# Performance work log

Hardware: AMD Instinct MI355X
Metric: run time of the kernel (lower is better)

Reference implementation:

```python
import jax, jax.numpy as jnp
import numpy as np

IN_F, OUT_F, NG = 2048, 8192, 16
EPS = 1e-5

def setup_inputs() -> dict:
    key = jax.random.key(0)
    k = jax.random.split(key, 6)
    x = jax.random.normal(k[0], (4096, IN_F), dtype=jnp.float32)
    W = jax.random.normal(k[1], (OUT_F, IN_F), dtype=jnp.float32) * (1.0 / np.sqrt(IN_F))
    b = jax.random.normal(k[2], (OUT_F,), dtype=jnp.float32) * 0.01
    gn_w = jnp.ones((OUT_F,), dtype=jnp.float32)
    gn_b = jnp.zeros((OUT_F,), dtype=jnp.float32)
    mult_w = jax.random.normal(k[3], (OUT_F,), dtype=jnp.float32)
    return {"x": x, "W": W, "b": b, "gn_w": gn_w, "gn_b": gn_b, "mult_w": mult_w}

def reference(x, W, b, gn_w, gn_b, mult_w):
    B = x.shape[0]
    y = x @ W.T + b  # [B, OUT_F]
    g = y.reshape(B, NG, OUT_F // NG)
    mean = jnp.mean(g, axis=-1, keepdims=True)
    var = jnp.mean(jnp.square(g - mean), axis=-1, keepdims=True)
    n = ((g - mean) * jax.lax.rsqrt(var + EPS)).reshape(B, OUT_F)
    n = n * gn_w + gn_b
    s1 = n * jax.nn.sigmoid(n)
    m = s1 * mult_w
    return m * jax.nn.sigmoid(m)
```

## Files before the change

### kernel.cpp

```cpp
#include <hip/hip_runtime.h>

#define M_DIM 4096
#define N_DIM 8192
#define K_DIM 2048
#define NGRP 16
#define GSZ 512
#define EPSV 1e-5f

#define NX (M_DIM * K_DIM)
#define NW (N_DIM * K_DIM)
#define NY ((size_t)M_DIM * N_DIM)

typedef __attribute__((ext_vector_type(8))) short bf16x8;
typedef __attribute__((ext_vector_type(4))) float f32x4;
typedef __attribute__((ext_vector_type(8))) short shortx8;

__device__ __forceinline__ float b2f(short u) {
    union { unsigned u32; float f; } c;
    c.u32 = ((unsigned)(unsigned short)u) << 16;
    return c.f;
}

__device__ __forceinline__ short f2b(float f) {
    union { float f; unsigned u; } c; c.f = f;
    unsigned r = (c.u + 0x7fffu + ((c.u >> 16) & 1u)) >> 16;
    return (short)r;
}

__global__ __launch_bounds__(256) void convert_kernel(
    const float* __restrict__ x, const float* __restrict__ W,
    short* __restrict__ dst)
{
    const size_t base = ((size_t)blockIdx.x * 256 + threadIdx.x) * 32;
    const float* src = (base < NX) ? (x + base) : (W + (base - NX));
    f32x4 v[8];
#pragma unroll
    for (int c = 0; c < 8; ++c) v[c] = *(const f32x4*)(src + c * 4);
#pragma unroll
    for (int c = 0; c < 4; ++c) {
        shortx8 o;
#pragma unroll
        for (int j = 0; j < 4; ++j) {
            o[j]     = f2b(v[2 * c][j]);
            o[j + 4] = f2b(v[2 * c + 1][j]);
        }
        *(shortx8*)(dst + base + c * 8) = o;
    }
}

#define BKS 32
#define NTILES (K_DIM / BKS)

__global__ __launch_bounds__(512, 2) void gemm256_bf16_kernel(
    const short* __restrict__ A, const short* __restrict__ W, short* __restrict__ C)
{
    __shared__ __align__(16) short lds[4 * 16384];

    const int tid  = threadIdx.x;
    const int lane = tid & 63;
    const int wave = tid >> 6;
    const int wr   = wave >> 2;
    const int wc   = wave & 3;
    const int blockRow = blockIdx.y * 256;
    const int blockCol = blockIdx.x * 256;

    const int q0 = tid, q1 = tid + 512;
    const int sr0 = q0 >> 2, sc0 = (q0 & 3) ^ (sr0 & 3);
    const int sr1 = q1 >> 2, sc1 = (q1 & 3) ^ (sr1 & 3);
    const short* gA0 = A + (size_t)(blockRow + sr0) * K_DIM + sc0 * 8;
    const short* gA1 = A + (size_t)(blockRow + sr1) * K_DIM + sc1 * 8;
    const short* gB0 = W + (size_t)(blockCol + sr0) * K_DIM + sc0 * 8;
    const short* gB1 = W + (size_t)(blockCol + sr1) * K_DIM + sc1 * 8;

    const int fr    = lane & 15;
    const int pbyte = ((lane >> 4) ^ (fr & 3)) * 16;
    const int aBase = (wr * 128 + fr) * 64 + pbyte;
    const int bBase = (wc * 64  + fr) * 64 + pbyte;

    f32x4 acc[8][4] = {};

    auto stageT = [&](int t) {
        short* dA = lds + (t & 3) * 16384;
        short* dB = dA + 8192;
        const int ko = t * BKS;
        __builtin_amdgcn_global_load_lds(
            (const __attribute__((address_space(1))) void*)(gA0 + ko),
            (__attribute__((address_space(3))) void*)(dA + q0 * 8), 16, 0, 0);
        __builtin_amdgcn_global_load_lds(
            (const __attribute__((address_space(1))) void*)(gB0 + ko),
            (__attribute__((address_space(3))) void*)(dB + q0 * 8), 16, 0, 0);
        __builtin_amdgcn_global_load_lds(
            (const __attribute__((address_space(1))) void*)(gA1 + ko),
            (__attribute__((address_space(3))) void*)(dA + q1 * 8), 16, 0, 0);
        __builtin_amdgcn_global_load_lds(
            (const __attribute__((address_space(1))) void*)(gB1 + ko),
            (__attribute__((address_space(3))) void*)(dB + q1 * 8), 16, 0, 0);
    };

    stageT(0); stageT(1); stageT(2);

    for (int t = 0; t < NTILES; ++t) {
        __builtin_amdgcn_s_barrier();
        __builtin_amdgcn_sched_barrier(0);
        if (t + 3 < NTILES) {
            stageT(t + 3);
            asm volatile("s_waitcnt vmcnt(12)" ::: "memory");
        } else if (t + 2 < NTILES) {
            asm volatile("s_waitcnt vmcnt(8)" ::: "memory");
        } else if (t + 1 < NTILES) {
            asm volatile("s_waitcnt vmcnt(4)" ::: "memory");
        } else {
            asm volatile("s_waitcnt vmcnt(0)" ::: "memory");
        }
        __builtin_amdgcn_s_barrier();
        __builtin_amdgcn_sched_barrier(0);

        const char* bufA = (const char*)lds + (t & 3) * 32768;
        const char* bufB = bufA + 16384;
        bf16x8 af[8], bfv[4];
#pragma unroll
        for (int i = 0; i < 8; ++i)
            af[i] = *(const bf16x8*)(bufA + aBase + i * 1024);
#pragma unroll
        for (int j = 0; j < 4; ++j)
            bfv[j] = *(const bf16x8*)(bufB + bBase + j * 1024);

        __builtin_amdgcn_s_setprio(1);
#pragma unroll
        for (int i = 0; i < 8; ++i)
#pragma unroll
            for (int j = 0; j < 4; ++j)
                acc[i][j] = __builtin_amdgcn_mfma_f32_16x16x32_bf16(
                    af[i], bfv[j], acc[i][j], 0, 0, 0);
        __builtin_amdgcn_s_setprio(0);
    }

    const int er = (lane >> 4) * 4;
    const int ec = lane & 15;
#pragma unroll
    for (int i = 0; i < 8; ++i) {
        const int rr = blockRow + wr * 128 + i * 16 + er;
#pragma unroll
        for (int j = 0; j < 4; ++j) {
            const int cc = blockCol + wc * 64 + j * 16 + ec;
#pragma unroll
            for (int r = 0; r < 4; ++r)
                C[(size_t)(rr + r) * N_DIM + cc] = f2b(acc[i][j][r]);
        }
    }
}

__global__ __launch_bounds__(256) void gn_silu_bf16_kernel(
    const short* __restrict__ Y,
    const float* __restrict__ bias,
    const float* __restrict__ gnw,
    const float* __restrict__ gnb,
    const float* __restrict__ mw,
    float* __restrict__ out)
{
    const int lane = threadIdx.x & 63;
    const int wave = threadIdx.x >> 6;
    const unsigned gid = blockIdx.x * 4u + wave;
    const unsigned row = gid >> 4;
    const unsigned grp = gid & 15;
    const int col = grp * GSZ + lane * 8;
    const size_t off = (size_t)row * N_DIM + col;

    bf16x8 v = *(const bf16x8*)(Y + off);
    f32x4 b0 = *(const f32x4*)(bias + col);
    f32x4 b1 = *(const f32x4*)(bias + col + 4);

    float y[8];
    float s = 0.f, s2 = 0.f;
#pragma unroll
    for (int j = 0; j < 8; ++j) {
        y[j] = b2f(v[j]) + (j < 4 ? b0[j] : b1[j - 4]);
        s  += y[j];
        s2 += y[j] * y[j];
    }
#pragma unroll
    for (int d = 1; d < 64; d <<= 1) {
        s  += __shfl_xor(s,  d, 64);
        s2 += __shfl_xor(s2, d, 64);
    }
    const float mean = s * (1.0f / GSZ);
    const float var  = s2 * (1.0f / GSZ) - mean * mean;
    const float inv  = rsqrtf(var + EPSV);

    f32x4 w0 = *(const f32x4*)(gnw + col);
    f32x4 w1 = *(const f32x4*)(gnw + col + 4);
    f32x4 g0 = *(const f32x4*)(gnb + col);
    f32x4 g1 = *(const f32x4*)(gnb + col + 4);
    f32x4 m0 = *(const f32x4*)(mw + col);
    f32x4 m1 = *(const f32x4*)(mw + col + 4);

    f32x4 o0, o1;
#pragma unroll
    for (int j = 0; j < 8; ++j) {
        float gwv = j < 4 ? w0[j] : w1[j - 4];
        float gbv = j < 4 ? g0[j] : g1[j - 4];
        float mwv = j < 4 ? m0[j] : m1[j - 4];
        float n  = (y[j] - mean) * inv * gwv + gbv;
        float s1 = n / (1.f + __expf(-n));
        float m  = s1 * mwv;
        float r  = m / (1.f + __expf(-m));
        if (j < 4) o0[j] = r; else o1[j - 4] = r;
    }
    *(f32x4*)(out + off)     = o0;
    *(f32x4*)(out + off + 4) = o1;
}

__global__ __launch_bounds__(256) void gemm_bt_f32_kernel(
    const float* __restrict__ A, const float* __restrict__ W, float* __restrict__ C)
{
    __shared__ __align__(16) short ldsA[128 * 32];
    __shared__ __align__(16) short ldsB[128 * 32];

    const int tid  = threadIdx.x;
    const int lane = tid & 63;
    const int wave = tid >> 6;
    const int blockRow = blockIdx.y * 128;
    const int blockCol = blockIdx.x * 128;
    const int srow = tid >> 1;
    const int scol = (tid & 1) * 16;
    const int wm  = (wave >> 1) * 64;
    const int wn  = (wave & 1) * 64;
    const int fr  = lane & 15;
    const int fko = (lane >> 4) * 8;

    f32x4 acc[4][4] = {};
    const size_t aRowOff = (size_t)(blockRow + srow) * K_DIM;
    const size_t wRowOff = (size_t)(blockCol + srow) * K_DIM;

    for (int k0 = 0; k0 < K_DIM; k0 += 32) {
        f32x4 va0 = *(const f32x4*)(A + aRowOff + k0 + scol);
        f32x4 va1 = *(const f32x4*)(A + aRowOff + k0 + scol + 4);
        f32x4 va2 = *(const f32x4*)(A + aRowOff + k0 + scol + 8);
        f32x4 va3 = *(const f32x4*)(A + aRowOff + k0 + scol + 12);
        f32x4 vb0 = *(const f32x4*)(W + wRowOff + k0 + scol);
        f32x4 vb1 = *(const f32x4*)(W + wRowOff + k0 + scol + 4);
        f32x4 vb2 = *(const f32x4*)(W + wRowOff + k0 + scol + 8);
        f32x4 vb3 = *(const f32x4*)(W + wRowOff + k0 + scol + 12);
        bf16x8 a0, a1, b0, b1;
#pragma unroll
        for (int j = 0; j < 4; ++j) {
            a0[j] = f2b(va0[j]); a0[j + 4] = f2b(va1[j]);
            a1[j] = f2b(va2[j]); a1[j + 4] = f2b(va3[j]);
            b0[j] = f2b(vb0[j]); b0[j + 4] = f2b(vb1[j]);
            b1[j] = f2b(vb2[j]); b1[j + 4] = f2b(vb3[j]);
        }
        *(bf16x8*)(ldsA + srow * 32 + scol)     = a0;
        *(bf16x8*)(ldsA + srow * 32 + scol + 8) = a1;
        *(bf16x8*)(ldsB + srow * 32 + scol)     = b0;
        *(bf16x8*)(ldsB + srow * 32 + scol + 8) = b1;
        __syncthreads();

        bf16x8 af[4], bfv[4];
#pragma unroll
        for (int i = 0; i < 4; ++i) {
            af[i]  = *(const bf16x8*)(ldsA + (wm + i * 16 + fr) * 32 + fko);
            bfv[i] = *(const bf16x8*)(ldsB + (wn + i * 16 + fr) * 32 + fko);
        }
#pragma unroll
        for (int i = 0; i < 4; ++i)
#pragma unroll
            for (int j = 0; j < 4; ++j)
                acc[i][j] = __builtin_amdgcn_mfma_f32_16x16x32_bf16(
                    af[i], bfv[j], acc[i][j], 0, 0, 0);
        __syncthreads();
    }

    const int er = (lane >> 4) * 4;
    const int ec = lane & 15;
#pragma unroll
    for (int i = 0; i < 4; ++i) {
        const int r0 = blockRow + wm + i * 16 + er;
#pragma unroll
        for (int j = 0; j < 4; ++j) {
            const int c0 = blockCol + wn + j * 16 + ec;
#pragma unroll
            for (int r = 0; r < 4; ++r)
                C[(size_t)(r0 + r) * N_DIM + c0] = acc[i][j][r];
        }
    }
}

__global__ __launch_bounds__(256) void gn_silu_f32_kernel(
    float* __restrict__ Y,
    const float* __restrict__ bias,
    const float* __restrict__ gnw,
    const float* __restrict__ gnb,
    const float* __restrict__ mw)
{
    const int lane = threadIdx.x & 63;
    const int wave = threadIdx.x >> 6;
    const unsigned gid = blockIdx.x * 4u + wave;
    const unsigned row = gid >> 4;
    const unsigned grp = gid & 15;
    const int col = grp * GSZ + lane * 8;
    const size_t off = (size_t)row * N_DIM + col;

    f32x4 v0 = *(const f32x4*)(Y + off);
    f32x4 v1 = *(const f32x4*)(Y + off + 4);
    f32x4 b0 = *(const f32x4*)(bias + col);
    f32x4 b1 = *(const f32x4*)(bias + col + 4);

    float y[8];
    float s = 0.f, s2 = 0.f;
#pragma unroll
    for (int j = 0; j < 8; ++j) {
        y[j] = (j < 4 ? v0[j] + b0[j] : v1[j - 4] + b1[j - 4]);
        s += y[j]; s2 += y[j] * y[j];
    }
#pragma unroll
    for (int d = 1; d < 64; d <<= 1) {
        s  += __shfl_xor(s,  d, 64);
        s2 += __shfl_xor(s2, d, 64);
    }
    const float mean = s * (1.0f / GSZ);
    const float var  = s2 * (1.0f / GSZ) - mean * mean;
    const float inv  = rsqrtf(var + EPSV);

    f32x4 w0 = *(const f32x4*)(gnw + col);
    f32x4 w1 = *(const f32x4*)(gnw + col + 4);
    f32x4 g0 = *(const f32x4*)(gnb + col);
    f32x4 g1 = *(const f32x4*)(gnb + col + 4);
    f32x4 m0 = *(const f32x4*)(mw + col);
    f32x4 m1 = *(const f32x4*)(mw + col + 4);

    f32x4 o0, o1;
#pragma unroll
    for (int j = 0; j < 8; ++j) {
        float gwv = j < 4 ? w0[j] : w1[j - 4];
        float gbv = j < 4 ? g0[j] : g1[j - 4];
        float mwv = j < 4 ? m0[j] : m1[j - 4];
        float n  = (y[j] - mean) * inv * gwv + gbv;
        float s1 = n / (1.f + __expf(-n));
        float m  = s1 * mwv;
        float r  = m / (1.f + __expf(-m));
        if (j < 4) o0[j] = r; else o1[j - 4] = r;
    }
    *(f32x4*)(Y + off)     = o0;
    *(f32x4*)(Y + off + 4) = o1;
}

extern "C" void kernel_launch(void* const* d_in, const int* in_sizes, int n_in,
                              void* d_out, int out_size, void* d_ws, size_t ws_size,
                              hipStream_t stream)
{
    const float* x   = (const float*)d_in[0];
    const float* W   = (const float*)d_in[1];
    const float* b   = (const float*)d_in[2];
    const float* gnw = (const float*)d_in[3];
    const float* gnb = (const float*)d_in[4];
    const float* mw  = (const float*)d_in[5];
    float* out = (float*)d_out;

    const size_t need = ((size_t)NX + NW + NY) * sizeof(short);
    const int ngroups = M_DIM * NGRP;

    if (ws_size >= need) {
        short* xb = (short*)d_ws;
        short* Wb = xb + NX;
        short* yb = Wb + NW;

        convert_kernel<<<(NX + NW) / (256 * 32), 256, 0, stream>>>(x, W, xb);
        dim3 g256(N_DIM / 256, M_DIM / 256);
        gemm256_bf16_kernel<<<g256, 512, 0, stream>>>(xb, Wb, yb);
        gn_silu_bf16_kernel<<<ngroups / 4, 256, 0, stream>>>(yb, b, gnw, gnb, mw, out);
    } else {
        dim3 ggrid(N_DIM / 128, M_DIM / 128);
        gemm_bt_f32_kernel<<<ggrid, 256, 0, stream>>>(x, W, out);
        gn_silu_f32_kernel<<<ngroups / 4, 256, 0, stream>>>(out, b, gnw, gnb, mw);
    }
}
```

Before: 381.4 us.

## Double-buffer MFMA fragments in registers and retune LDS swizzle in bf16 GEMM

The K-loop now prefetches the next tile's A/B fragments from LDS into a second register set while MFMAs run on the current set. It ping-pongs between two 12-fragment buffers, with adjusted vmcnt/lgkmcnt waits and barriers. The LDS XOR swizzle now uses a row>>1 pattern on both the global-to-LDS write side and the fragment read side, aimed at reducing bank conflicts. Global addressing switches from precomputed pointers to 32-bit offsets. This hides LDS read latency behind MFMA work, at the cost of roughly 12 extra vector registers per thread, which may pressure occupancy at launch_bounds(512,2).

```diff
diff --git a/kernel.cpp b/kernel.cpp
--- a/kernel.cpp
+++ b/kernel.cpp
@@ -65,15 +65,15 @@
     const int blockCol = blockIdx.x * 256;
 
     const int q0 = tid, q1 = tid + 512;
-    const int sr0 = q0 >> 2, sc0 = (q0 & 3) ^ (sr0 & 3);
-    const int sr1 = q1 >> 2, sc1 = (q1 & 3) ^ (sr1 & 3);
-    const short* gA0 = A + (size_t)(blockRow + sr0) * K_DIM + sc0 * 8;
-    const short* gA1 = A + (size_t)(blockRow + sr1) * K_DIM + sc1 * 8;
-    const short* gB0 = W + (size_t)(blockCol + sr0) * K_DIM + sc0 * 8;
-    const short* gB1 = W + (size_t)(blockCol + sr1) * K_DIM + sc1 * 8;
+    const int sr0 = q0 >> 2, sc0 = (q0 & 3) ^ ((q0 >> 3) & 3);
+    const int sr1 = q1 >> 2, sc1 = (q1 & 3) ^ ((q1 >> 3) & 3);
+    const int offA0 = (blockRow + sr0) * K_DIM + sc0 * 8;
+    const int offA1 = (blockRow + sr1) * K_DIM + sc1 * 8;
+    const int offB0 = (blockCol + sr0) * K_DIM + sc0 * 8;
+    const int offB1 = (blockCol + sr1) * K_DIM + sc1 * 8;
 
     const int fr    = lane & 15;
-    const int pbyte = ((lane >> 4) ^ (fr & 3)) * 16;
+    const int pbyte = ((lane >> 4) ^ ((fr >> 1) & 3)) * 16;
     const int aBase = (wr * 128 + fr) * 64 + pbyte;
     const int bBase = (wc * 64  + fr) * 64 + pbyte;
 
@@ -84,55 +84,75 @@
         short* dB = dA + 8192;
         const int ko = t * BKS;
         __builtin_amdgcn_global_load_lds(
-            (const __attribute__((address_space(1))) void*)(gA0 + ko),
+            (const __attribute__((address_space(1))) void*)(A + offA0 + ko),
             (__attribute__((address_space(3))) void*)(dA + q0 * 8), 16, 0, 0);
         __builtin_amdgcn_global_load_lds(
-            (const __attribute__((address_space(1))) void*)(gB0 + ko),
+            (const __attribute__((address_space(1))) void*)(W + offB0 + ko),
             (__attribute__((address_space(3))) void*)(dB + q0 * 8), 16, 0, 0);
         __builtin_amdgcn_global_load_lds(
-            (const __attribute__((address_space(1))) void*)(gA1 + ko),
+            (const __attribute__((address_space(1))) void*)(A + offA1 + ko),
             (__attribute__((address_space(3))) void*)(dA + q1 * 8), 16, 0, 0);
         __builtin_amdgcn_global_load_lds(
-            (const __attribute__((address_space(1))) void*)(gB1 + ko),
+            (const __attribute__((address_space(1))) void*)(W + offB1 + ko),
             (__attribute__((address_space(3))) void*)(dB + q1 * 8), 16, 0, 0);
     };
 
-    stageT(0); stageT(1); stageT(2);
-
-    for (int t = 0; t < NTILES; ++t) {
+    auto ldfrags = [&](int t, bf16x8 (&f)[12]) {
+        const char* bufA = (const char*)lds + (t & 3) * 32768;
+        const char* bufB = bufA + 16384;
+#pragma unroll
+        for (int i = 0; i < 8; ++i)
+            f[i] = *(const bf16x8*)(bufA + aBase + i * 1024);
+#pragma unroll
+        for (int j = 0; j < 4; ++j)
+            f[8 + j] = *(const bf16x8*)(bufB + bBase + j * 1024);
+    };
+
+    auto domfma = [&](bf16x8 (&f)[12]) {
+        __builtin_amdgcn_s_setprio(1);
+#pragma unroll
+        for (int i = 0; i < 8; ++i)
+#pragma unroll
+            for (int j = 0; j < 4; ++j)
+                acc[i][j] = __builtin_amdgcn_mfma_f32_16x16x32_bf16(
+                    f[i], f[8 + j], acc[i][j], 0, 0, 0);
+        __builtin_amdgcn_s_setprio(0);
+    };
+
+    auto step = [&](int t, bf16x8 (&cur)[12], bf16x8 (&nxt)[12]) {
+        if (t + 3 < NTILES) {
+            stageT(t + 3);
+            asm volatile("s_waitcnt vmcnt(8)" ::: "memory");
+        } else if (t + 2 < NTILES) {
+            asm volatile("s_waitcnt vmcnt(4)" ::: "memory");
+        } else if (t + 1 < NTILES) {
+            asm volatile("s_waitcnt vmcnt(0)" ::: "memory");
+        }
         __builtin_amdgcn_s_barrier();
         __builtin_amdgcn_sched_barrier(0);
-        if (t + 3 < NTILES) {
-            stageT(t + 3);
-            asm volatile("s_waitcnt vmcnt(12)" ::: "memory");
-        } else if (t + 2 < NTILES) {
-            asm volatile("s_waitcnt vmcnt(8)" ::: "memory");
-        } else if (t + 1 < NTILES) {
-            asm volatile("s_waitcnt vmcnt(4)" ::: "memory");
+        if (t + 1 < NTILES) {
+            ldfrags(t + 1, nxt);
+            asm volatile("s_waitcnt lgkmcnt(12)" ::: "memory");
         } else {
-            asm volatile("s_waitcnt vmcnt(0)" ::: "memory");
-        }
+            asm volatile("s_waitcnt lgkmcnt(0)" ::: "memory");
+        }
+        __builtin_amdgcn_sched_barrier(0);
         __builtin_amdgcn_s_barrier();
         __builtin_amdgcn_sched_barrier(0);
-
-        const char* bufA = (const char*)lds + (t & 3) * 32768;
-        const char* bufB = bufA + 16384;
-        bf16x8 af[8], bfv[4];
-#pragma unroll
-        for (int i = 0; i < 8; ++i)
-            af[i] = *(const bf16x8*)(bufA + aBase + i * 1024);
-#pragma unroll
-        for (int j = 0; j < 4; ++j)
-            bfv[j] = *(const bf16x8*)(bufB + bBase + j * 1024);
-
-        __builtin_amdgcn_s_setprio(1);
-#pragma unroll
-        for (int i = 0; i < 8; ++i)
-#pragma unroll
-            for (int j = 0; j < 4; ++j)
-                acc[i][j] = __builtin_amdgcn_mfma_f32_16x16x32_bf16(
-                    af[i], bfv[j], acc[i][j], 0, 0, 0);
-        __builtin_amdgcn_s_setprio(0);
+        domfma(cur);
+    };
+
+    bf16x8 fE[12], fO[12];
+
+    stageT(0); stageT(1); stageT(2);
+    asm volatile("s_waitcnt vmcnt(8)" ::: "memory");
+    __builtin_amdgcn_s_barrier();
+    __builtin_amdgcn_sched_barrier(0);
+    ldfrags(0, fE);
+
+    for (int t = 0; t < NTILES; t += 2) {
+        step(t,     fE, fO);
+        step(t + 1, fO, fE);
     }
 
     const int er = (lane >> 4) * 4;
```

Measured after the change: 369.8 us. 1.03x faster.
